# Performance work log

Hardware: AMD Instinct MI355X
Metric: run time of the kernel (lower is better)

## Reference

```python
import jax, jax.numpy as jnp
import numpy as np

D_MODEL = 512
SEQ_LEN = 2048
S = 32  # local window size
BATCH = 2


def setup_inputs() -> dict:
    key = jax.random.key(0)
    ks = jax.random.split(key, 12)
    shp = (SEQ_LEN, BATCH, D_MODEL)
    return {
        "query": jax.random.normal(ks[0], shp, jnp.float32),
        "key": jax.random.normal(ks[1], shp, jnp.float32),
        "value": jax.random.normal(ks[2], shp, jnp.float32),
        "Wq": jax.random.normal(ks[3], (D_MODEL, D_MODEL), jnp.float32) * 0.02,
        "bq": jax.random.normal(ks[4], (D_MODEL,), jnp.float32) * 0.01,
        "Wk": jax.random.normal(ks[5], (D_MODEL, D_MODEL), jnp.float32) * 0.02,
        "bk": jax.random.normal(ks[6], (D_MODEL,), jnp.float32) * 0.01,
        "Wv": jax.random.normal(ks[7], (D_MODEL, D_MODEL), jnp.float32) * 0.02,
        "bv": jax.random.normal(ks[8], (D_MODEL,), jnp.float32) * 0.01,
        "pos_bias": jax.random.normal(ks[9], (SEQ_LEN, SEQ_LEN), jnp.float32) * 0.02,
        "Wo": jax.random.normal(ks[10], (D_MODEL, D_MODEL), jnp.float32) * 0.02,
        "bo": jax.random.normal(ks[11], (D_MODEL,), jnp.float32) * 0.01,
    }


def _aft_local(query, key, value, Wq, bq, Wk, bk, Wv, bv, pos_bias, Wo, bo):
    T, B, D = query.shape
    q = query @ Wq.T + bq  # [T,B,D]
    k = key @ Wk.T + bk
    v = value @ Wv.T + bv
    pb = pos_bias[:T, :T]

    # max_logit: elementwise max of per-dim key max and (key + col-max of pos_bias) max,
    # then batch index 0 (faithful to original `[0]` indexing) -> shape [D]
    max_logit = jnp.maximum(k.max(axis=0),
                            (k + pb.max(axis=0)[:, None, None]).max(axis=0))[0]

    # out-of-window running sums: tokens t' <= t - S contribute exp(k) (no pos bias)
    ek = jnp.exp(k - max_logit)                 # [T,B,D]
    cs_num = jnp.cumsum(ek * v, axis=0)
    cs_den = jnp.cumsum(ek, axis=0)
    t_arr = jnp.arange(T)
    prefix_idx = jnp.clip(t_arr - S, 0, T - 1)
    has_prefix = (t_arr >= S)[:, None, None]
    num_out = jnp.where(has_prefix, cs_num[prefix_idx], 0.0)
    den_out = jnp.where(has_prefix, cs_den[prefix_idx], 0.0)

    # in-window part: t' in [max(0, t-S+1), t] with pos_bias[t, t']
    j = jnp.arange(S)
    idx_raw = t_arr[:, None] - S + 1 + j[None, :]   # [T,S]
    valid = (idx_raw >= 0).astype(k.dtype)
    idx = jnp.clip(idx_raw, 0, T - 1)
    k_win = k[idx]                                  # [T,S,B,D]
    v_win = v[idx]                                  # [T,S,B,D]
    pb_win = pb[t_arr[:, None], idx]                # [T,S]
    exp_l = jnp.exp(k_win + pb_win[:, :, None, None] - max_logit) * valid[:, :, None, None]
    num_in = (exp_l * v_win).sum(axis=1)            # [T,B,D]
    den_in = exp_l.sum(axis=1)

    y = jax.nn.sigmoid(q) * (num_out + num_in) / (den_out + den_in)
    return y @ Wo.T + bo


def reference(query, key, value, Wq, bq, Wk, bk, Wv, bv, pos_bias, Wo, bo):
    return _aft_local(query, key, value, Wq, bq, Wk, bk, Wv, bv, pos_bias, Wo, bo)
```

## Files before the change

### kernel.cpp

```cpp
#include <hip/hip_runtime.h>
#include <hip/hip_bf16.h>

#define TT 2048
#define BB 2
#define DD 512
#define BD (BB*DD)
#define SS 32
#define MR (TT*BB)
#define NE (TT*BB*DD)
#define CH 32

typedef __bf16 bf16x8 __attribute__((ext_vector_type(8)));
typedef float f32x4 __attribute__((ext_vector_type(4)));
typedef float f32x2 __attribute__((ext_vector_type(2)));

__device__ __forceinline__ void async_copy16(void* lds, const void* gptr) {
    __builtin_amdgcn_global_load_lds(
        (const __attribute__((address_space(1))) void*)gptr,
        (__attribute__((address_space(3))) void*)lds,
        16, 0, 0);
}

#define MFMA16(a,b,c) __builtin_amdgcn_mfma_f32_16x16x32_bf16((a),(b),(c),0,0,0)

__global__ __launch_bounds__(256) void cast_all(
    const float* __restrict__ s0, const float* __restrict__ s1, const float* __restrict__ s2,
    const float* __restrict__ w0, const float* __restrict__ w1,
    const float* __restrict__ w2, const float* __restrict__ w3,
    __hip_bfloat16* __restrict__ d0, __hip_bfloat16* __restrict__ d1, __hip_bfloat16* __restrict__ d2,
    __hip_bfloat16* __restrict__ e0, __hip_bfloat16* __restrict__ e1,
    __hip_bfloat16* __restrict__ e2, __hip_bfloat16* __restrict__ e3)
{
    int b = blockIdx.x;
    const float* s;
    __hip_bfloat16* d;
    size_t i;
    if (b < 6144) {
        int which = b >> 11;
        s = which == 0 ? s0 : (which == 1 ? s1 : s2);
        d = which == 0 ? d0 : (which == 1 ? d1 : d2);
        i = ((size_t)(b & 2047) * 256 + threadIdx.x) * 4;
    } else {
        int b2 = b - 6144;
        int which = b2 >> 8;
        s = which == 0 ? w0 : (which == 1 ? w1 : (which == 2 ? w2 : w3));
        d = which == 0 ? e0 : (which == 1 ? e1 : (which == 2 ? e2 : e3));
        i = ((size_t)(b2 & 255) * 256 + threadIdx.x) * 4;
    }
    float4 f = *(const float4*)(s + i);
    union { __hip_bfloat16 h[4]; ushort4 u; } cv;
    cv.h[0] = __float2bfloat16(f.x); cv.h[1] = __float2bfloat16(f.y);
    cv.h[2] = __float2bfloat16(f.z); cv.h[3] = __float2bfloat16(f.w);
    *(ushort4*)((unsigned short*)d + i) = cv.u;
}

__global__ __launch_bounds__(256) void gemm_qkv(
    const __hip_bfloat16* __restrict__ qb, const __hip_bfloat16* __restrict__ kb,
    const __hip_bfloat16* __restrict__ vb,
    const __hip_bfloat16* __restrict__ Wqb, const __hip_bfloat16* __restrict__ Wkb,
    const __hip_bfloat16* __restrict__ Wvb,
    const float* __restrict__ bq, const float* __restrict__ bk,
    const float* __restrict__ bv,
    float* __restrict__ qout, float* __restrict__ ekn,
    float* __restrict__ part)
{
    __shared__ char smem[49152];
    const int tid = threadIdx.x;
    const int lane = tid & 63;
    const int wv = tid >> 6;
    const int wave_m = wv >> 1, wave_n = wv & 1;
    const int m0 = blockIdx.y * 64, n0 = blockIdx.x * 64;
    const int kq = lane >> 4, rr = lane & 15;

    if (blockIdx.z == 0) {
        f32x4 acc[2][2] = {};
        const __hip_bfloat16* Arow = qb + (size_t)(m0 + lane) * DD + wv * 8;
        const __hip_bfloat16* Wrow = Wqb + (size_t)(n0 + lane) * DD + wv * 8;
        async_copy16(smem + 0*8192 +        wv*1024, Arow + 0);
        async_copy16(smem + 0*8192 + 4096 + wv*1024, Wrow + 0);
        async_copy16(smem + 1*8192 +        wv*1024, Arow + 32);
        async_copy16(smem + 1*8192 + 4096 + wv*1024, Wrow + 32);
        asm volatile("s_waitcnt vmcnt(2)" ::: "memory");
        __builtin_amdgcn_s_barrier();
        #pragma unroll
        for (int it = 0; it < 16; ++it) {
            if (it + 2 < 16) {
                char* nb = smem + ((it + 2) % 3) * 8192;
                async_copy16(nb +        wv*1024, Arow + (it+2)*32);
                async_copy16(nb + 4096 + wv*1024, Wrow + (it+2)*32);
            }
            const char* cb = smem + (it % 3) * 8192;
            bf16x8 a0 = *(const bf16x8*)(cb + kq*1024 + (wave_m*32 +  0 + rr)*16);
            bf16x8 a1 = *(const bf16x8*)(cb + kq*1024 + (wave_m*32 + 16 + rr)*16);
            bf16x8 w0 = *(const bf16x8*)(cb + 4096 + kq*1024 + (wave_n*32 +  0 + rr)*16);
            bf16x8 w1 = *(const bf16x8*)(cb + 4096 + kq*1024 + (wave_n*32 + 16 + rr)*16);
            acc[0][0] = MFMA16(a0, w0, acc[0][0]);
            acc[0][1] = MFMA16(a0, w1, acc[0][1]);
            acc[1][0] = MFMA16(a1, w0, acc[1][0]);
            acc[1][1] = MFMA16(a1, w1, acc[1][1]);
            if (it < 15) {
                if (it < 14) asm volatile("s_waitcnt vmcnt(2) lgkmcnt(0)" ::: "memory");
                else         asm volatile("s_waitcnt vmcnt(0) lgkmcnt(0)" ::: "memory");
                __builtin_amdgcn_s_barrier();
            }
        }
        #pragma unroll
        for (int ms = 0; ms < 2; ++ms)
            #pragma unroll
            for (int ns = 0; ns < 2; ++ns) {
                int n = n0 + wave_n*32 + ns*16 + rr;
                float bn = bq[n];
                #pragma unroll
                for (int r = 0; r < 4; ++r) {
                    int m = m0 + wave_m*32 + ms*16 + kq*4 + r;
                    qout[(size_t)m * DD + n] = acc[ms][ns][r] + bn;
                }
            }
    } else {
        f32x4 acck[2][2] = {}, accv[2][2] = {};
        const __hip_bfloat16* AKrow = kb + (size_t)(m0 + lane) * DD + wv * 8;
        const __hip_bfloat16* WKrow = Wkb + (size_t)(n0 + lane) * DD + wv * 8;
        const __hip_bfloat16* AVrow = vb + (size_t)(m0 + lane) * DD + wv * 8;
        const __hip_bfloat16* WVrow = Wvb + (size_t)(n0 + lane) * DD + wv * 8;
        #pragma unroll
        for (int pt = 0; pt < 2; ++pt) {
            char* nb = smem + pt * 16384;
            async_copy16(nb +         wv*1024, AKrow + pt*32);
            async_copy16(nb +  4096 + wv*1024, WKrow + pt*32);
            async_copy16(nb +  8192 + wv*1024, AVrow + pt*32);
            async_copy16(nb + 12288 + wv*1024, WVrow + pt*32);
        }
        asm volatile("s_waitcnt vmcnt(4)" ::: "memory");
        __builtin_amdgcn_s_barrier();
        #pragma unroll
        for (int it = 0; it < 16; ++it) {
            if (it + 2 < 16) {
                char* nb = smem + ((it + 2) % 3) * 16384;
                async_copy16(nb +         wv*1024, AKrow + (it+2)*32);
                async_copy16(nb +  4096 + wv*1024, WKrow + (it+2)*32);
                async_copy16(nb +  8192 + wv*1024, AVrow + (it+2)*32);
                async_copy16(nb + 12288 + wv*1024, WVrow + (it+2)*32);
            }
            const char* cb = smem + (it % 3) * 16384;
            bf16x8 ak0 = *(const bf16x8*)(cb +         kq*1024 + (wave_m*32 +  0 + rr)*16);
            bf16x8 ak1 = *(const bf16x8*)(cb +         kq*1024 + (wave_m*32 + 16 + rr)*16);
            bf16x8 bk0 = *(const bf16x8*)(cb +  4096 + kq*1024 + (wave_n*32 +  0 + rr)*16);
            bf16x8 bk1 = *(const bf16x8*)(cb +  4096 + kq*1024 + (wave_n*32 + 16 + rr)*16);
            bf16x8 av0 = *(const bf16x8*)(cb +  8192 + kq*1024 + (wave_m*32 +  0 + rr)*16);
            bf16x8 av1 = *(const bf16x8*)(cb +  8192 + kq*1024 + (wave_m*32 + 16 + rr)*16);
            bf16x8 bv0 = *(const bf16x8*)(cb + 12288 + kq*1024 + (wave_n*32 +  0 + rr)*16);
            bf16x8 bv1 = *(const bf16x8*)(cb + 12288 + kq*1024 + (wave_n*32 + 16 + rr)*16);
            acck[0][0] = MFMA16(ak0, bk0, acck[0][0]);
            acck[0][1] = MFMA16(ak0, bk1, acck[0][1]);
            acck[1][0] = MFMA16(ak1, bk0, acck[1][0]);
            acck[1][1] = MFMA16(ak1, bk1, acck[1][1]);
            accv[0][0] = MFMA16(av0, bv0, accv[0][0]);
            accv[0][1] = MFMA16(av0, bv1, accv[0][1]);
            accv[1][0] = MFMA16(av1, bv0, accv[1][0]);
            accv[1][1] = MFMA16(av1, bv1, accv[1][1]);
            if (it < 15) {
                if (it < 14) asm volatile("s_waitcnt vmcnt(4) lgkmcnt(0)" ::: "memory");
                else         asm volatile("s_waitcnt vmcnt(0) lgkmcnt(0)" ::: "memory");
                __builtin_amdgcn_s_barrier();
            }
        }
        float sd[2][2] = {{0.f,0.f},{0.f,0.f}};
        float sn[2][2] = {{0.f,0.f},{0.f,0.f}};
        #pragma unroll
        for (int ms = 0; ms < 2; ++ms)
            #pragma unroll
            for (int ns = 0; ns < 2; ++ns) {
                int n = n0 + wave_n*32 + ns*16 + rr;
                float bkn = bk[n], bvn = bv[n];
                #pragma unroll
                for (int r = 0; r < 4; ++r) {
                    int m = m0 + wave_m*32 + ms*16 + kq*4 + r;
                    float e  = expf(acck[ms][ns][r] + bkn);
                    float nv = e * (accv[ms][ns][r] + bvn);
                    float2 st; st.x = e; st.y = nv;
                    *(float2*)&ekn[((size_t)m * DD + n) * 2] = st;
                    sd[ns][r & 1] += e;
                    sn[ns][r & 1] += nv;
                }
            }
        #pragma unroll
        for (int ns = 0; ns < 2; ++ns)
            #pragma unroll
            for (int par = 0; par < 2; ++par) {
                sd[ns][par] += __shfl_xor(sd[ns][par], 16, 64);
                sd[ns][par] += __shfl_xor(sd[ns][par], 32, 64);
                sn[ns][par] += __shfl_xor(sn[ns][par], 16, 64);
                sn[ns][par] += __shfl_xor(sn[ns][par], 32, 64);
            }
        __syncthreads();
        float* red = (float*)smem;
        if (lane < 16) {
            #pragma unroll
            for (int ns = 0; ns < 2; ++ns) {
                int c2 = wave_n*32 + ns*16 + rr;
                red[(0*2 + wave_m)*64 + c2] = sd[ns][0];
                red[(1*2 + wave_m)*64 + c2] = sd[ns][1];
                red[(2*2 + wave_m)*64 + c2] = sn[ns][0];
                red[(3*2 + wave_m)*64 + c2] = sn[ns][1];
            }
        }
        __syncthreads();
        {
            int which = tid >> 6;
            int c2 = tid & 63;
            float s = red[(which*2 + 0)*64 + c2] + red[(which*2 + 1)*64 + c2];
            int b = which & 1;
            int sel = which >> 1;
            part[((size_t)blockIdx.y * BD + b*512 + n0 + c2) * 2 + sel] = s;
        }
    }
}

__global__ __launch_bounds__(256, 1) void scan_part(
    const float* __restrict__ part, float* __restrict__ pref)
{
    const int col = blockIdx.x * 256 + threadIdx.x;
    f32x2 run = {0.f, 0.f};
    #pragma unroll
    for (int p0 = 0; p0 < 64; p0 += 8) {
        f32x2 v[8];
        #pragma unroll
        for (int u = 0; u < 8; ++u)
            v[u] = *(const f32x2*)&part[((size_t)(p0 + u) * BD + col) * 2];
        #pragma unroll
        for (int u = 0; u < 8; ++u) {
            *(f32x2*)&pref[((size_t)(p0 + u) * BD + col) * 2] = run;
            run += v[u];
        }
    }
}

__global__ __launch_bounds__(256, 3) void fused_window(
    const float* __restrict__ q, const float* __restrict__ ekn,
    const float* __restrict__ pref, const float* __restrict__ pb,
    __hip_bfloat16* __restrict__ yb)
{
    __shared__ float Et[64 * 64 * 2];
    __shared__ float wl[CH][SS];
    const int tid = threadIdx.x;
    const int chunk = blockIdx.y;
    const int t0 = chunk * CH;
    const int col0 = blockIdx.x * 64;
    const int c = tid & 63;
    const int sg = tid >> 6;
    const int s0 = sg * 8;

    {
        const int ub = tid >> 5;
        const int cp = tid & 31;
        #pragma unroll
        for (int j = 0; j < 8; ++j) {
            int u = ub + j * 8;
            int t = t0 - 32 + u;
            if (t >= 0) {
                const void* g = (const void*)(ekn + ((size_t)t * BD + col0 + cp * 2) * 2);
                async_copy16((char*)Et + (tid >> 6) * 1024 + j * 4096, g);
            }
        }
        if (chunk == 0) {
            f32x4 z = {0.f, 0.f, 0.f, 0.f};
            #pragma unroll
            for (int j = 0; j < 4; ++j)
                *(f32x4*)((char*)Et + tid * 16 + j * 4096) = z;
        }
    }

    #pragma unroll
    for (int i = 0; i < (CH * SS) / 256; ++i) {
        int idx = tid + i * 256;
        int tl = idx >> 5, jj = idx & 31;
        int t = t0 + tl;
        int u2 = t - (SS - 1) + jj;
        float w = 0.f;
        if (u2 >= 0) w = expf(pb[(size_t)t * TT + u2]);
        wl[tl][jj] = w;
    }

    float qv[8];
    #pragma unroll
    for (int k = 0; k < 8; ++k)
        qv[k] = q[(size_t)(t0 + s0 + k) * BD + col0 + c];
    f32x2 P = *(const f32x2*)&pref[((size_t)chunk * BD + col0 + c) * 2];

    __syncthreads();

    f32x2 ring[39];
    #pragma unroll
    for (int i = 0; i < 39; ++i)
        ring[i] = *(const f32x2*)&Et[((s0 + 1 + i) * 64 + c) * 2];

    f32x2 cs = P;
    #pragma unroll
    for (int u = 0; u < 31; ++u)
        if (u >= s0) cs -= ring[u - s0];

    #pragma unroll
    for (int k = 0; k < 8; ++k) {
        int s = s0 + k;
        if (k > 0) cs += ring[k - 1];
        f32x2 acc = cs;
        #pragma unroll
        for (int j4 = 0; j4 < 8; ++j4) {
            float4 w4 = *(const float4*)&wl[s][j4 * 4];
            acc += w4.x * ring[k + j4*4 + 0];
            acc += w4.y * ring[k + j4*4 + 1];
            acc += w4.z * ring[k + j4*4 + 2];
            acc += w4.w * ring[k + j4*4 + 3];
        }
        float sig = 1.f / (1.f + expf(-qv[k]));
        yb[(size_t)(t0 + s) * BD + col0 + c] = __float2bfloat16(sig * acc.y / acc.x);
    }
}

__global__ __launch_bounds__(256) void gemm_out(
    const __hip_bfloat16* __restrict__ yb, const __hip_bfloat16* __restrict__ Wob,
    const float* __restrict__ bo, float* __restrict__ out)
{
    __shared__ char smem[24576];
    const int tid = threadIdx.x;
    const int lane = tid & 63;
    const int wv = tid >> 6;
    const int wave_m = wv >> 1, wave_n = wv & 1;
    const int m0 = blockIdx.y * 64, n0 = blockIdx.x * 64;
    const int kq = lane >> 4, rr = lane & 15;

    f32x4 acc[2][2] = {};
    const __hip_bfloat16* Arow = yb + (size_t)(m0 + lane) * DD + wv * 8;
    const __hip_bfloat16* Wrow = Wob + (size_t)(n0 + lane) * DD + wv * 8;

    async_copy16(smem + 0*8192 +        wv*1024, Arow + 0);
    async_copy16(smem + 0*8192 + 4096 + wv*1024, Wrow + 0);
    async_copy16(smem + 1*8192 +        wv*1024, Arow + 32);
    async_copy16(smem + 1*8192 + 4096 + wv*1024, Wrow + 32);
    asm volatile("s_waitcnt vmcnt(2)" ::: "memory");
    __builtin_amdgcn_s_barrier();
    #pragma unroll
    for (int it = 0; it < 16; ++it) {
        if (it + 2 < 16) {
            char* nb = smem + ((it + 2) % 3) * 8192;
            async_copy16(nb +        wv*1024, Arow + (it+2)*32);
            async_copy16(nb + 4096 + wv*1024, Wrow + (it+2)*32);
        }
        const char* cb = smem + (it % 3) * 8192;
        bf16x8 a0 = *(const bf16x8*)(cb + kq*1024 + (wave_m*32 +  0 + rr)*16);
        bf16x8 a1 = *(const bf16x8*)(cb + kq*1024 + (wave_m*32 + 16 + rr)*16);
        bf16x8 w0 = *(const bf16x8*)(cb + 4096 + kq*1024 + (wave_n*32 +  0 + rr)*16);
        bf16x8 w1 = *(const bf16x8*)(cb + 4096 + kq*1024 + (wave_n*32 + 16 + rr)*16);
        acc[0][0] = MFMA16(a0, w0, acc[0][0]);
        acc[0][1] = MFMA16(a0, w1, acc[0][1]);
        acc[1][0] = MFMA16(a1, w0, acc[1][0]);
        acc[1][1] = MFMA16(a1, w1, acc[1][1]);
        if (it < 15) {
            if (it < 14) asm volatile("s_waitcnt vmcnt(2) lgkmcnt(0)" ::: "memory");
            else         asm volatile("s_waitcnt vmcnt(0) lgkmcnt(0)" ::: "memory");
            __builtin_amdgcn_s_barrier();
        }
    }
    #pragma unroll
    for (int ms = 0; ms < 2; ++ms)
        #pragma unroll
        for (int ns = 0; ns < 2; ++ns) {
            int n = n0 + wave_n*32 + ns*16 + rr;
            float bn = bo[n];
            #pragma unroll
            for (int r = 0; r < 4; ++r) {
                int m = m0 + wave_m*32 + ms*16 + kq*4 + r;
                out[(size_t)m * DD + n] = acc[ms][ns][r] + bn;
            }
        }
}

extern "C" void kernel_launch(void* const* d_in, const int* in_sizes, int n_in,
                              void* d_out, int out_size, void* d_ws, size_t ws_size,
                              hipStream_t stream) {
    const float* query = (const float*)d_in[0];
    const float* key   = (const float*)d_in[1];
    const float* value = (const float*)d_in[2];
    const float* Wq    = (const float*)d_in[3];
    const float* bq    = (const float*)d_in[4];
    const float* Wk    = (const float*)d_in[5];
    const float* bk    = (const float*)d_in[6];
    const float* Wv    = (const float*)d_in[7];
    const float* bv    = (const float*)d_in[8];
    const float* pb    = (const float*)d_in[9];
    const float* Wo    = (const float*)d_in[10];
    const float* bo    = (const float*)d_in[11];
    float* out = (float*)d_out;

    float* ws = (float*)d_ws;
    float* q    = ws;
    float* ekn  = ws + (size_t)NE;
    float* part = ws + (size_t)3 * NE;
    float* pref = part + 131072;
    __hip_bfloat16* bfb = (__hip_bfloat16*)(pref + 131072);
    __hip_bfloat16* qb  = bfb;
    __hip_bfloat16* kb  = bfb + (size_t)NE;
    __hip_bfloat16* vb  = bfb + (size_t)2 * NE;
    __hip_bfloat16* yb  = bfb + (size_t)3 * NE;
    __hip_bfloat16* Wqb = bfb + (size_t)4 * NE;
    __hip_bfloat16* Wkb = Wqb + 262144;
    __hip_bfloat16* Wvb = Wkb + 262144;
    __hip_bfloat16* Wob = Wvb + 262144;

    cast_all<<<7168, 256, 0, stream>>>(query, key, value, Wq, Wk, Wv, Wo,
                                       qb, kb, vb, Wqb, Wkb, Wvb, Wob);

    gemm_qkv<<<dim3(DD / 64, MR / 64, 2), 256, 0, stream>>>(
        qb, kb, vb, Wqb, Wkb, Wvb, bq, bk, bv,
        q, ekn, part);

    scan_part<<<4, 256, 0, stream>>>(part, pref);

    fused_window<<<dim3(BD / 64, TT / CH), 256, 0, stream>>>(
        q, ekn, pref, pb, yb);

    gemm_out<<<dim3(DD / 64, MR / 64), 256, 0, stream>>>(yb, Wob, bo, out);
}
```

Measured before the change: 190.3 us.

## Fuse fp32-to-bf16 casts into GEMM loaders and drop separate scan kernel

Removes the standalone cast kernel: the GEMMs now load fp32 inputs and weights into registers, convert them to bf16 and store them to LDS in a register-staged double-buffered pipeline, replacing the async global-to-LDS triple buffering. The prefix-scan kernel is removed, and each fused_window block instead sums the chunk partials below its position, with a small LDS reduction across its four thread groups. The sigmoid on q moves into the QKV GEMM epilogue. This saves two kernel launches and the bf16 intermediate round trips, but the GEMMs now read twice the bytes, lose the async-copy overlap, and fused_window does redundant partial-sum reads.

After: 216.9 us. 1.14x slower.

```diff
diff --git a/kernel.cpp b/kernel.cpp
--- a/kernel.cpp
+++ b/kernel.cpp
@@ -11,6 +11,7 @@
 #define CH 32
 
 typedef __bf16 bf16x8 __attribute__((ext_vector_type(8)));
+typedef short short8 __attribute__((ext_vector_type(8)));
 typedef float f32x4 __attribute__((ext_vector_type(4)));
 typedef float f32x2 __attribute__((ext_vector_type(2)));
 
@@ -23,86 +24,58 @@
 
 #define MFMA16(a,b,c) __builtin_amdgcn_mfma_f32_16x16x32_bf16((a),(b),(c),0,0,0)
 
-__global__ __launch_bounds__(256) void cast_all(
-    const float* __restrict__ s0, const float* __restrict__ s1, const float* __restrict__ s2,
-    const float* __restrict__ w0, const float* __restrict__ w1,
-    const float* __restrict__ w2, const float* __restrict__ w3,
-    __hip_bfloat16* __restrict__ d0, __hip_bfloat16* __restrict__ d1, __hip_bfloat16* __restrict__ d2,
-    __hip_bfloat16* __restrict__ e0, __hip_bfloat16* __restrict__ e1,
-    __hip_bfloat16* __restrict__ e2, __hip_bfloat16* __restrict__ e3)
-{
-    int b = blockIdx.x;
-    const float* s;
-    __hip_bfloat16* d;
-    size_t i;
-    if (b < 6144) {
-        int which = b >> 11;
-        s = which == 0 ? s0 : (which == 1 ? s1 : s2);
-        d = which == 0 ? d0 : (which == 1 ? d1 : d2);
-        i = ((size_t)(b & 2047) * 256 + threadIdx.x) * 4;
-    } else {
-        int b2 = b - 6144;
-        int which = b2 >> 8;
-        s = which == 0 ? w0 : (which == 1 ? w1 : (which == 2 ? w2 : w3));
-        d = which == 0 ? e0 : (which == 1 ? e1 : (which == 2 ? e2 : e3));
-        i = ((size_t)(b2 & 255) * 256 + threadIdx.x) * 4;
-    }
-    float4 f = *(const float4*)(s + i);
-    union { __hip_bfloat16 h[4]; ushort4 u; } cv;
-    cv.h[0] = __float2bfloat16(f.x); cv.h[1] = __float2bfloat16(f.y);
-    cv.h[2] = __float2bfloat16(f.z); cv.h[3] = __float2bfloat16(f.w);
-    *(ushort4*)((unsigned short*)d + i) = cv.u;
+__device__ __forceinline__ void cvt_store16(void* dst, float4 a, float4 b) {
+    union { __hip_bfloat16 h[8]; short8 s; } u;
+    u.h[0] = __float2bfloat16(a.x); u.h[1] = __float2bfloat16(a.y);
+    u.h[2] = __float2bfloat16(a.z); u.h[3] = __float2bfloat16(a.w);
+    u.h[4] = __float2bfloat16(b.x); u.h[5] = __float2bfloat16(b.y);
+    u.h[6] = __float2bfloat16(b.z); u.h[7] = __float2bfloat16(b.w);
+    *(short8*)dst = u.s;
 }
 
 __global__ __launch_bounds__(256) void gemm_qkv(
-    const __hip_bfloat16* __restrict__ qb, const __hip_bfloat16* __restrict__ kb,
-    const __hip_bfloat16* __restrict__ vb,
-    const __hip_bfloat16* __restrict__ Wqb, const __hip_bfloat16* __restrict__ Wkb,
-    const __hip_bfloat16* __restrict__ Wvb,
+    const float* __restrict__ query, const float* __restrict__ key,
+    const float* __restrict__ value,
+    const float* __restrict__ Wq, const float* __restrict__ Wk,
+    const float* __restrict__ Wv,
     const float* __restrict__ bq, const float* __restrict__ bk,
     const float* __restrict__ bv,
     float* __restrict__ qout, float* __restrict__ ekn,
     float* __restrict__ part)
 {
-    __shared__ char smem[49152];
+    __shared__ char smem[32768];
     const int tid = threadIdx.x;
     const int lane = tid & 63;
     const int wv = tid >> 6;
     const int wave_m = wv >> 1, wave_n = wv & 1;
     const int m0 = blockIdx.y * 64, n0 = blockIdx.x * 64;
     const int kq = lane >> 4, rr = lane & 15;
+    char* const wr = smem + wv * 1024 + lane * 16;
 
     if (blockIdx.z == 0) {
+        const float* A = query + (size_t)(m0 + lane) * DD + wv * 8;
+        const float* W = Wq    + (size_t)(n0 + lane) * DD + wv * 8;
         f32x4 acc[2][2] = {};
-        const __hip_bfloat16* Arow = qb + (size_t)(m0 + lane) * DD + wv * 8;
-        const __hip_bfloat16* Wrow = Wqb + (size_t)(n0 + lane) * DD + wv * 8;
-        async_copy16(smem + 0*8192 +        wv*1024, Arow + 0);
-        async_copy16(smem + 0*8192 + 4096 + wv*1024, Wrow + 0);
-        async_copy16(smem + 1*8192 +        wv*1024, Arow + 32);
-        async_copy16(smem + 1*8192 + 4096 + wv*1024, Wrow + 32);
-        asm volatile("s_waitcnt vmcnt(2)" ::: "memory");
-        __builtin_amdgcn_s_barrier();
+        float4 a0, a1, w0, w1;
+#define LD0(t) { a0 = *(const float4*)(A + (t)*32); a1 = *(const float4*)(A + (t)*32 + 4); \
+                 w0 = *(const float4*)(W + (t)*32); w1 = *(const float4*)(W + (t)*32 + 4); }
+#define ST0(b) { cvt_store16(wr + (b)*8192, a0, a1); cvt_store16(wr + (b)*8192 + 4096, w0, w1); }
+        LD0(0); ST0(0); LD0(1);
+        __syncthreads();
         #pragma unroll
         for (int it = 0; it < 16; ++it) {
-            if (it + 2 < 16) {
-                char* nb = smem + ((it + 2) % 3) * 8192;
-                async_copy16(nb +        wv*1024, Arow + (it+2)*32);
-                async_copy16(nb + 4096 + wv*1024, Wrow + (it+2)*32);
-            }
-            const char* cb = smem + (it % 3) * 8192;
-            bf16x8 a0 = *(const bf16x8*)(cb + kq*1024 + (wave_m*32 +  0 + rr)*16);
-            bf16x8 a1 = *(const bf16x8*)(cb + kq*1024 + (wave_m*32 + 16 + rr)*16);
-            bf16x8 w0 = *(const bf16x8*)(cb + 4096 + kq*1024 + (wave_n*32 +  0 + rr)*16);
-            bf16x8 w1 = *(const bf16x8*)(cb + 4096 + kq*1024 + (wave_n*32 + 16 + rr)*16);
-            acc[0][0] = MFMA16(a0, w0, acc[0][0]);
-            acc[0][1] = MFMA16(a0, w1, acc[0][1]);
-            acc[1][0] = MFMA16(a1, w0, acc[1][0]);
-            acc[1][1] = MFMA16(a1, w1, acc[1][1]);
-            if (it < 15) {
-                if (it < 14) asm volatile("s_waitcnt vmcnt(2) lgkmcnt(0)" ::: "memory");
-                else         asm volatile("s_waitcnt vmcnt(0) lgkmcnt(0)" ::: "memory");
-                __builtin_amdgcn_s_barrier();
-            }
+            const char* cb = smem + (it & 1) * 8192;
+            bf16x8 fa0 = *(const bf16x8*)(cb + kq*1024 + (wave_m*32 +  0 + rr)*16);
+            bf16x8 fa1 = *(const bf16x8*)(cb + kq*1024 + (wave_m*32 + 16 + rr)*16);
+            bf16x8 fw0 = *(const bf16x8*)(cb + 4096 + kq*1024 + (wave_n*32 +  0 + rr)*16);
+            bf16x8 fw1 = *(const bf16x8*)(cb + 4096 + kq*1024 + (wave_n*32 + 16 + rr)*16);
+            acc[0][0] = MFMA16(fa0, fw0, acc[0][0]);
+            acc[0][1] = MFMA16(fa0, fw1, acc[0][1]);
+            acc[1][0] = MFMA16(fa1, fw0, acc[1][0]);
+            acc[1][1] = MFMA16(fa1, fw1, acc[1][1]);
+            if (it + 1 < 16) ST0((it + 1) & 1);
+            if (it + 2 < 16) LD0(it + 2);
+            if (it < 15) __syncthreads();
         }
         #pragma unroll
         for (int ms = 0; ms < 2; ++ms)
@@ -113,56 +86,49 @@
                 #pragma unroll
                 for (int r = 0; r < 4; ++r) {
                     int m = m0 + wave_m*32 + ms*16 + kq*4 + r;
-                    qout[(size_t)m * DD + n] = acc[ms][ns][r] + bn;
+                    float x = acc[ms][ns][r] + bn;
+                    qout[(size_t)m * DD + n] = 1.f / (1.f + expf(-x));
                 }
             }
     } else {
+        const float* AK = key   + (size_t)(m0 + lane) * DD + wv * 8;
+        const float* WK = Wk    + (size_t)(n0 + lane) * DD + wv * 8;
+        const float* AV = value + (size_t)(m0 + lane) * DD + wv * 8;
+        const float* WV = Wv    + (size_t)(n0 + lane) * DD + wv * 8;
         f32x4 acck[2][2] = {}, accv[2][2] = {};
-        const __hip_bfloat16* AKrow = kb + (size_t)(m0 + lane) * DD + wv * 8;
-        const __hip_bfloat16* WKrow = Wkb + (size_t)(n0 + lane) * DD + wv * 8;
-        const __hip_bfloat16* AVrow = vb + (size_t)(m0 + lane) * DD + wv * 8;
-        const __hip_bfloat16* WVrow = Wvb + (size_t)(n0 + lane) * DD + wv * 8;
-        #pragma unroll
-        for (int pt = 0; pt < 2; ++pt) {
-            char* nb = smem + pt * 16384;
-            async_copy16(nb +         wv*1024, AKrow + pt*32);
-            async_copy16(nb +  4096 + wv*1024, WKrow + pt*32);
-            async_copy16(nb +  8192 + wv*1024, AVrow + pt*32);
-            async_copy16(nb + 12288 + wv*1024, WVrow + pt*32);
-        }
-        asm volatile("s_waitcnt vmcnt(4)" ::: "memory");
-        __builtin_amdgcn_s_barrier();
+        float4 ak0, ak1, wk0, wk1, av0, av1, wv0, wv1;
+#define LD1(t) { ak0 = *(const float4*)(AK + (t)*32); ak1 = *(const float4*)(AK + (t)*32 + 4); \
+                 wk0 = *(const float4*)(WK + (t)*32); wk1 = *(const float4*)(WK + (t)*32 + 4); \
+                 av0 = *(const float4*)(AV + (t)*32); av1 = *(const float4*)(AV + (t)*32 + 4); \
+                 wv0 = *(const float4*)(WV + (t)*32); wv1 = *(const float4*)(WV + (t)*32 + 4); }
+#define ST1(b) { cvt_store16(wr + (b)*16384,         ak0, ak1); \
+                 cvt_store16(wr + (b)*16384 +  4096, wk0, wk1); \
+                 cvt_store16(wr + (b)*16384 +  8192, av0, av1); \
+                 cvt_store16(wr + (b)*16384 + 12288, wv0, wv1); }
+        LD1(0); ST1(0); LD1(1);
+        __syncthreads();
         #pragma unroll
         for (int it = 0; it < 16; ++it) {
-            if (it + 2 < 16) {
-                char* nb = smem + ((it + 2) % 3) * 16384;
-                async_copy16(nb +         wv*1024, AKrow + (it+2)*32);
-                async_copy16(nb +  4096 + wv*1024, WKrow + (it+2)*32);
-                async_copy16(nb +  8192 + wv*1024, AVrow + (it+2)*32);
-                async_copy16(nb + 12288 + wv*1024, WVrow + (it+2)*32);
-            }
-            const char* cb = smem + (it % 3) * 16384;
-            bf16x8 ak0 = *(const bf16x8*)(cb +         kq*1024 + (wave_m*32 +  0 + rr)*16);
-            bf16x8 ak1 = *(const bf16x8*)(cb +         kq*1024 + (wave_m*32 + 16 + rr)*16);
-            bf16x8 bk0 = *(const bf16x8*)(cb +  4096 + kq*1024 + (wave_n*32 +  0 + rr)*16);
-            bf16x8 bk1 = *(const bf16x8*)(cb +  4096 + kq*1024 + (wave_n*32 + 16 + rr)*16);
-            bf16x8 av0 = *(const bf16x8*)(cb +  8192 + kq*1024 + (wave_m*32 +  0 + rr)*16);
-            bf16x8 av1 = *(const bf16x8*)(cb +  8192 + kq*1024 + (wave_m*32 + 16 + rr)*16);
-            bf16x8 bv0 = *(const bf16x8*)(cb + 12288 + kq*1024 + (wave_n*32 +  0 + rr)*16);
-            bf16x8 bv1 = *(const bf16x8*)(cb + 12288 + kq*1024 + (wave_n*32 + 16 + rr)*16);
-            acck[0][0] = MFMA16(ak0, bk0, acck[0][0]);
-            acck[0][1] = MFMA16(ak0, bk1, acck[0][1]);
-            acck[1][0] = MFMA16(ak1, bk0, acck[1][0]);
-            acck[1][1] = MFMA16(ak1, bk1, acck[1][1]);
-            accv[0][0] = MFMA16(av0, bv0, accv[0][0]);
-            accv[0][1] = MFMA16(av0, bv1, accv[0][1]);
-            accv[1][0] = MFMA16(av1, bv0, accv[1][0]);
-            accv[1][1] = MFMA16(av1, bv1, accv[1][1]);
-            if (it < 15) {
-                if (it < 14) asm volatile("s_waitcnt vmcnt(4) lgkmcnt(0)" ::: "memory");
-                else         asm volatile("s_waitcnt vmcnt(0) lgkmcnt(0)" ::: "memory");
-                __builtin_amdgcn_s_barrier();
-            }
+            const char* cb = smem + (it & 1) * 16384;
+            bf16x8 fk0 = *(const bf16x8*)(cb +         kq*1024 + (wave_m*32 +  0 + rr)*16);
+            bf16x8 fk1 = *(const bf16x8*)(cb +         kq*1024 + (wave_m*32 + 16 + rr)*16);
+            bf16x8 gk0 = *(const bf16x8*)(cb +  4096 + kq*1024 + (wave_n*32 +  0 + rr)*16);
+            bf16x8 gk1 = *(const bf16x8*)(cb +  4096 + kq*1024 + (wave_n*32 + 16 + rr)*16);
+            bf16x8 fv0 = *(const bf16x8*)(cb +  8192 + kq*1024 + (wave_m*32 +  0 + rr)*16);
+            bf16x8 fv1 = *(const bf16x8*)(cb +  8192 + kq*1024 + (wave_m*32 + 16 + rr)*16);
+            bf16x8 gv0 = *(const bf16x8*)(cb + 12288 + kq*1024 + (wave_n*32 +  0 + rr)*16);
+            bf16x8 gv1 = *(const bf16x8*)(cb + 12288 + kq*1024 + (wave_n*32 + 16 + rr)*16);
+            acck[0][0] = MFMA16(fk0, gk0, acck[0][0]);
+            acck[0][1] = MFMA16(fk0, gk1, acck[0][1]);
+            acck[1][0] = MFMA16(fk1, gk0, acck[1][0]);
+            acck[1][1] = MFMA16(fk1, gk1, acck[1][1]);
+            accv[0][0] = MFMA16(fv0, gv0, accv[0][0]);
+            accv[0][1] = MFMA16(fv0, gv1, accv[0][1]);
+            accv[1][0] = MFMA16(fv1, gv0, accv[1][0]);
+            accv[1][1] = MFMA16(fv1, gv1, accv[1][1]);
+            if (it + 1 < 16) ST1((it + 1) & 1);
+            if (it + 2 < 16) LD1(it + 2);
+            if (it < 15) __syncthreads();
         }
         float sd[2][2] = {{0.f,0.f},{0.f,0.f}};
         float sn[2][2] = {{0.f,0.f},{0.f,0.f}};
@@ -216,32 +182,14 @@
     }
 }
 
-__global__ __launch_bounds__(256, 1) void scan_part(
-    const float* __restrict__ part, float* __restrict__ pref)
-{
-    const int col = blockIdx.x * 256 + threadIdx.x;
-    f32x2 run = {0.f, 0.f};
-    #pragma unroll
-    for (int p0 = 0; p0 < 64; p0 += 8) {
-        f32x2 v[8];
-        #pragma unroll
-        for (int u = 0; u < 8; ++u)
-            v[u] = *(const f32x2*)&part[((size_t)(p0 + u) * BD + col) * 2];
-        #pragma unroll
-        for (int u = 0; u < 8; ++u) {
-            *(f32x2*)&pref[((size_t)(p0 + u) * BD + col) * 2] = run;
-            run += v[u];
-        }
-    }
-}
-
 __global__ __launch_bounds__(256, 3) void fused_window(
-    const float* __restrict__ q, const float* __restrict__ ekn,
-    const float* __restrict__ pref, const float* __restrict__ pb,
+    const float* __restrict__ qf, const float* __restrict__ ekn,
+    const float* __restrict__ part, const float* __restrict__ pb,
     __hip_bfloat16* __restrict__ yb)
 {
     __shared__ float Et[64 * 64 * 2];
     __shared__ float wl[CH][SS];
+    __shared__ float red[4 * 64 * 2];
     const int tid = threadIdx.x;
     const int chunk = blockIdx.y;
     const int t0 = chunk * CH;
@@ -251,11 +199,10 @@
     const int s0 = sg * 8;
 
     {
-        const int ub = tid >> 5;
         const int cp = tid & 31;
         #pragma unroll
         for (int j = 0; j < 8; ++j) {
-            int u = ub + j * 8;
+            int u = (tid >> 5) + j * 8;
             int t = t0 - 32 + u;
             if (t >= 0) {
                 const void* g = (const void*)(ekn + ((size_t)t * BD + col0 + cp * 2) * 2);
@@ -284,10 +231,22 @@
     float qv[8];
     #pragma unroll
     for (int k = 0; k < 8; ++k)
-        qv[k] = q[(size_t)(t0 + s0 + k) * BD + col0 + c];
-    f32x2 P = *(const f32x2*)&pref[((size_t)chunk * BD + col0 + c) * 2];
+        qv[k] = qf[(size_t)(t0 + s0 + k) * BD + col0 + c];
+    f32x2 acc2 = {0.f, 0.f};
+    #pragma unroll
+    for (int j = 0; j < 16; ++j) {
+        int p = sg + 4 * j;
+        if (p < chunk)
+            acc2 += *(const f32x2*)&part[((size_t)p * BD + col0 + c) * 2];
+    }
+    *(f32x2*)&red[(sg * 64 + c) * 2] = acc2;
 
     __syncthreads();
+
+    f32x2 P = *(const f32x2*)&red[(0 * 64 + c) * 2];
+    P += *(const f32x2*)&red[(1 * 64 + c) * 2];
+    P += *(const f32x2*)&red[(2 * 64 + c) * 2];
+    P += *(const f32x2*)&red[(3 * 64 + c) * 2];
 
     f32x2 ring[39];
     #pragma unroll
@@ -312,54 +271,46 @@
             acc += w4.z * ring[k + j4*4 + 2];
             acc += w4.w * ring[k + j4*4 + 3];
         }
-        float sig = 1.f / (1.f + expf(-qv[k]));
-        yb[(size_t)(t0 + s) * BD + col0 + c] = __float2bfloat16(sig * acc.y / acc.x);
+        yb[(size_t)(t0 + s) * BD + col0 + c] = __float2bfloat16(qv[k] * acc.y / acc.x);
     }
 }
 
 __global__ __launch_bounds__(256) void gemm_out(
-    const __hip_bfloat16* __restrict__ yb, const __hip_bfloat16* __restrict__ Wob,
+    const __hip_bfloat16* __restrict__ yb, const float* __restrict__ Wo,
     const float* __restrict__ bo, float* __restrict__ out)
 {
-    __shared__ char smem[24576];
+    __shared__ char smem[16384];
     const int tid = threadIdx.x;
     const int lane = tid & 63;
     const int wv = tid >> 6;
     const int wave_m = wv >> 1, wave_n = wv & 1;
     const int m0 = blockIdx.y * 64, n0 = blockIdx.x * 64;
     const int kq = lane >> 4, rr = lane & 15;
-
+    char* const wr = smem + wv * 1024 + lane * 16;
+
+    const __hip_bfloat16* A = yb + (size_t)(m0 + lane) * DD + wv * 8;
+    const float* W = Wo + (size_t)(n0 + lane) * DD + wv * 8;
     f32x4 acc[2][2] = {};
-    const __hip_bfloat16* Arow = yb + (size_t)(m0 + lane) * DD + wv * 8;
-    const __hip_bfloat16* Wrow = Wob + (size_t)(n0 + lane) * DD + wv * 8;
-
-    async_copy16(smem + 0*8192 +        wv*1024, Arow + 0);
-    async_copy16(smem + 0*8192 + 4096 + wv*1024, Wrow + 0);
-    async_copy16(smem + 1*8192 +        wv*1024, Arow + 32);
-    async_copy16(smem + 1*8192 + 4096 + wv*1024, Wrow + 32);
-    asm volatile("s_waitcnt vmcnt(2)" ::: "memory");
-    __builtin_amdgcn_s_barrier();
+    short8 ra; float4 w0, w1;
+#define LDO(t) { ra = *(const short8*)(A + (t)*32); \
+                 w0 = *(const float4*)(W + (t)*32); w1 = *(const float4*)(W + (t)*32 + 4); }
+#define STO(b) { *(short8*)(wr + (b)*8192) = ra; cvt_store16(wr + (b)*8192 + 4096, w0, w1); }
+    LDO(0); STO(0); LDO(1);
+    __syncthreads();
     #pragma unroll
     for (int it = 0; it < 16; ++it) {
-        if (it + 2 < 16) {
-            char* nb = smem + ((it + 2) % 3) * 8192;
-            async_copy16(nb +        wv*1024, Arow + (it+2)*32);
-            async_copy16(nb + 4096 + wv*1024, Wrow + (it+2)*32);
-        }
-        const char* cb = smem + (it % 3) * 8192;
-        bf16x8 a0 = *(const bf16x8*)(cb + kq*1024 + (wave_m*32 +  0 + rr)*16);
-        bf16x8 a1 = *(const bf16x8*)(cb + kq*1024 + (wave_m*32 + 16 + rr)*16);
-        bf16x8 w0 = *(const bf16x8*)(cb + 4096 + kq*1024 + (wave_n*32 +  0 + rr)*16);
-        bf16x8 w1 = *(const bf16x8*)(cb + 4096 + kq*1024 + (wave_n*32 + 16 + rr)*16);
-        acc[0][0] = MFMA16(a0, w0, acc[0][0]);
-        acc[0][1] = MFMA16(a0, w1, acc[0][1]);
-        acc[1][0] = MFMA16(a1, w0, acc[1][0]);
-        acc[1][1] = MFMA16(a1, w1, acc[1][1]);
-        if (it < 15) {
-            if (it < 14) asm volatile("s_waitcnt vmcnt(2) lgkmcnt(0)" ::: "memory");
-            else         asm volatile("s_waitcnt vmcnt(0) lgkmcnt(0)" ::: "memory");
-            __builtin_amdgcn_s_barrier();
-        }
+        const char* cb = smem + (it & 1) * 8192;
+        bf16x8 fa0 = *(const bf16x8*)(cb + kq*1024 + (wave_m*32 +  0 + rr)*16);
+        bf16x8 fa1 = *(const bf16x8*)(cb + kq*1024 + (wave_m*32 + 16 + rr)*16);
+        bf16x8 fw0 = *(const bf16x8*)(cb + 4096 + kq*1024 + (wave_n*32 +  0 + rr)*16);
+        bf16x8 fw1 = *(const bf16x8*)(cb + 4096 + kq*1024 + (wave_n*32 + 16 + rr)*16);
+        acc[0][0] = MFMA16(fa0, fw0, acc[0][0]);
+        acc[0][1] = MFMA16(fa0, fw1, acc[0][1]);
+        acc[1][0] = MFMA16(fa1, fw0, acc[1][0]);
+        acc[1][1] = MFMA16(fa1, fw1, acc[1][1]);
+        if (it + 1 < 16) STO((it + 1) & 1);
+        if (it + 2 < 16) LDO(it + 2);
+        if (it < 15) __syncthreads();
     }
     #pragma unroll
     for (int ms = 0; ms < 2; ++ms)
@@ -393,31 +344,17 @@
     float* out = (float*)d_out;
 
     float* ws = (float*)d_ws;
-    float* q    = ws;
+    float* qf   = ws;
     float* ekn  = ws + (size_t)NE;
     float* part = ws + (size_t)3 * NE;
-    float* pref = part + 131072;
-    __hip_bfloat16* bfb = (__hip_bfloat16*)(pref + 131072);
-    __hip_bfloat16* qb  = bfb;
-    __hip_bfloat16* kb  = bfb + (size_t)NE;
-    __hip_bfloat16* vb  = bfb + (size_t)2 * NE;
-    __hip_bfloat16* yb  = bfb + (size_t)3 * NE;
-    __hip_bfloat16* Wqb = bfb + (size_t)4 * NE;
-    __hip_bfloat16* Wkb = Wqb + 262144;
-    __hip_bfloat16* Wvb = Wkb + 262144;
-    __hip_bfloat16* Wob = Wvb + 262144;
-
-    cast_all<<<7168, 256, 0, stream>>>(query, key, value, Wq, Wk, Wv, Wo,
-                                       qb, kb, vb, Wqb, Wkb, Wvb, Wob);
+    __hip_bfloat16* yb = (__hip_bfloat16*)(part + 131072);
 
     gemm_qkv<<<dim3(DD / 64, MR / 64, 2), 256, 0, stream>>>(
-        qb, kb, vb, Wqb, Wkb, Wvb, bq, bk, bv,
-        q, ekn, part);
-
-    scan_part<<<4, 256, 0, stream>>>(part, pref);
+        query, key, value, Wq, Wk, Wv, bq, bk, bv,
+        qf, ekn, part);
 
     fused_window<<<dim3(BD / 64, TT / CH), 256, 0, stream>>>(
-        q, ekn, pref, pb, yb);
-
-    gemm_out<<<dim3(DD / 64, MR / 64), 256, 0, stream>>>(yb, Wob, bo, out);
-}
+        qf, ekn, part, pb, yb);
+
+    gemm_out<<<dim3(DD / 64, MR / 64), 256, 0, stream>>>(yb, Wo, bo, out);
+}
```
